# Kernel optimization log

Hardware: AMD Instinct MI355X
Metric: run time of the kernel (lower is better)

Reference implementation:

```python
import jax, jax.numpy as jnp
import numpy as np

NUM_CLASSES = 14  # centroids_pred has 14 centroids; target labels in [0,14)


def smooth(x):
    # smooth-L1: 0.5*x^2 if |x|<1 else |x|-0.5
    ax = jnp.abs(x)
    return jnp.where(ax < 1.0, 0.5 * x * x, ax - 0.5)


def setup_inputs() -> dict:
    key = jax.random.key(0)
    k1, k2, k3, k4, k5 = jax.random.split(key, 5)
    B, N, P = 32, 16384, 4096
    return {
        "displacement_pred": jax.random.normal(k1, (B, N), dtype=jnp.float32),
        "subsampled_points": jax.random.normal(k2, (B, 3, N), dtype=jnp.float32),
        "centroids_pred": jax.random.normal(k3, (B, 3, NUM_CLASSES), dtype=jnp.float32),
        "origin_points": jax.random.normal(k4, (B, 9, P), dtype=jnp.float32),
        "target": jax.random.randint(k5, (B, P), 0, NUM_CLASSES, dtype=jnp.int64),
    }


def reference(displacement_pred, subsampled_points, centroids_pred, origin_points, target):
    # origin_points: [B,9,P] -> xyz [B,P,3]
    xyz = jnp.transpose(origin_points, (0, 2, 1))[:, :, :3]
    # per-batch, per-class centroid means (get_centroids), vectorized via one-hot
    onehot = jax.nn.one_hot(target, NUM_CLASSES, dtype=xyz.dtype)       # [B,P,C]
    sums = jnp.einsum('bpc,bpd->bcd', onehot, xyz)                      # [B,C,3]
    counts = jnp.sum(onehot, axis=1)                                    # [B,C]
    cent_gt = sums / jnp.maximum(counts, 1.0)[:, :, None]               # [B,C,3]

    # distance estimate loss: nearest-GT-centroid distance per subsampled point
    sub = jnp.transpose(subsampled_points, (0, 2, 1))                   # [B,N,3]
    d2 = jnp.sum((sub[:, :, None, :] - cent_gt[:, None, :, :]) ** 2, -1)  # [B,N,C]
    dist = jnp.sqrt(jnp.min(d2, axis=-1))                               # [B,N]
    distance_loss = jnp.sum(smooth(displacement_pred - dist), axis=1)   # [B]

    # chamfer distance loss between predicted and GT centroids
    pred = jnp.transpose(centroids_pred, (0, 2, 1))                     # [B,Cp,3]
    D = jnp.sum((pred[:, :, None, :] - cent_gt[:, None, :, :]) ** 2, -1)  # [B,Cp,C]
    l1 = jnp.sum(jnp.min(D, axis=1), axis=-1)                           # [B]
    l2 = jnp.sum(jnp.min(D, axis=2), axis=-1)                           # [B]

    # separation loss: ratio of closest to 2nd-closest euclidean distance
    Dd = jnp.sqrt(D)                                                    # [B,Cp,C]
    closest2 = -jax.lax.top_k(-Dd, 2)[0]                                # [B,Cp,2] smallest two
    separation = jnp.sum(closest2[..., 0] / closest2[..., 1], axis=-1)  # [B]

    beta = 0.1
    return jnp.sum(distance_loss + l1 + l2 + beta * separation)
```

## Files before the change

kernel.cpp:

```cpp
#include <hip/hip_runtime.h>
#include <math.h>

#define NC 14
#define BB 32
#define NN 16384
#define PP 4096

#define WS_COUNTER 0
#define WS_DIST    64
#define WS_CENT    640
#define BLK_PER_B  8
#define NBLK_B     (BB * BLK_PER_B)

__global__ void centroids_kernel(const float* __restrict__ origin,
                                 const int*   __restrict__ target,
                                 float* __restrict__ ws) {
    const int b    = blockIdx.x / NC;
    const int c    = blockIdx.x % NC;
    const int tid  = threadIdx.x;
    const int lane = tid & 63;
    const int wave = tid >> 6;

    if (blockIdx.x == 0 && tid == 0) ((unsigned int*)ws)[WS_COUNTER] = 0u;

    const float* ob = origin + (size_t)b * 9 * PP;
    const int*   tb = target + (size_t)b * PP;

    float sx = 0.f, sy = 0.f, sz = 0.f, cnt = 0.f;
    const int p0 = tid * 4;
    #pragma unroll
    for (int it = 0; it < PP / 1024; ++it) {
        const int p = p0 + it * 1024;
        const int4   tv = *(const int4*)&tb[p];
        const float4 xv = *(const float4*)&ob[p];
        const float4 yv = *(const float4*)&ob[PP + p];
        const float4 zv = *(const float4*)&ob[2 * PP + p];
        float m0 = (tv.x == c) ? 1.f : 0.f;
        float m1 = (tv.y == c) ? 1.f : 0.f;
        float m2 = (tv.z == c) ? 1.f : 0.f;
        float m3 = (tv.w == c) ? 1.f : 0.f;
        sx = fmaf(m0, xv.x, fmaf(m1, xv.y, fmaf(m2, xv.z, fmaf(m3, xv.w, sx))));
        sy = fmaf(m0, yv.x, fmaf(m1, yv.y, fmaf(m2, yv.z, fmaf(m3, yv.w, sy))));
        sz = fmaf(m0, zv.x, fmaf(m1, zv.y, fmaf(m2, zv.z, fmaf(m3, zv.w, sz))));
        cnt += m0 + m1 + m2 + m3;
    }

    #pragma unroll
    for (int o = 32; o > 0; o >>= 1) {
        sx  += __shfl_down(sx, o);
        sy  += __shfl_down(sy, o);
        sz  += __shfl_down(sz, o);
        cnt += __shfl_down(cnt, o);
    }

    __shared__ float s_part[4][4];
    if (lane == 0) {
        s_part[wave][0] = sx; s_part[wave][1] = sy;
        s_part[wave][2] = sz; s_part[wave][3] = cnt;
    }
    __syncthreads();

    if (tid == 0) {
        float X = s_part[0][0] + s_part[1][0] + s_part[2][0] + s_part[3][0];
        float Y = s_part[0][1] + s_part[1][1] + s_part[2][1] + s_part[3][1];
        float Z = s_part[0][2] + s_part[1][2] + s_part[2][2] + s_part[3][2];
        float n = fmaxf(s_part[0][3] + s_part[1][3] + s_part[2][3] + s_part[3][3], 1.f);
        const int base = WS_CENT + (b * NC + c) * 3;
        ws[base + 0] = X / n;
        ws[base + 1] = Y / n;
        ws[base + 2] = Z / n;
    }
}

__global__ void distance_loss_kernel(const float* __restrict__ disp,
                                     const float* __restrict__ sub,
                                     const float* __restrict__ cpred,
                                     float* __restrict__ ws,
                                     float* __restrict__ out) {
    const int b   = blockIdx.x / BLK_PER_B;
    const int j   = blockIdx.x % BLK_PER_B;
    const int tid = threadIdx.x;

    __shared__ float s_cent[NC * 3];
    if (tid < NC * 3)
        s_cent[tid] = ws[WS_CENT + (size_t)b * NC * 3 + tid];
    __syncthreads();

    const int n0 = j * (NN / BLK_PER_B) + tid * 4;
    float sm = 0.f;
    #pragma unroll
    for (int it = 0; it < 2; ++it) {
        const int n = n0 + it * 1024;
        const float4 xv = *(const float4*)&sub[((size_t)b * 3 + 0) * NN + n];
        const float4 yv = *(const float4*)&sub[((size_t)b * 3 + 1) * NN + n];
        const float4 zv = *(const float4*)&sub[((size_t)b * 3 + 2) * NN + n];
        const float4 dv = *(const float4*)&disp[(size_t)b * NN + n];
        const float xs[4] = {xv.x, xv.y, xv.z, xv.w};
        const float ys[4] = {yv.x, yv.y, yv.z, yv.w};
        const float zs[4] = {zv.x, zv.y, zv.z, zv.w};
        const float ds[4] = {dv.x, dv.y, dv.z, dv.w};
        #pragma unroll
        for (int k = 0; k < 4; ++k) {
            float mn = 1e30f;
            #pragma unroll
            for (int c = 0; c < NC; ++c) {
                float dx = xs[k] - s_cent[c * 3 + 0];
                float dy = ys[k] - s_cent[c * 3 + 1];
                float dz = zs[k] - s_cent[c * 3 + 2];
                mn = fminf(mn, dx * dx + dy * dy + dz * dz);
            }
            float v  = ds[k] - sqrtf(mn);
            float av = fabsf(v);
            sm += (av < 1.f) ? 0.5f * v * v : (av - 0.5f);
        }
    }

    #pragma unroll
    for (int o = 32; o > 0; o >>= 1) sm += __shfl_down(sm, o);

    __shared__ float s_part[4];
    const int wave = tid >> 6;
    if ((tid & 63) == 0) s_part[wave] = sm;

    __shared__ float s_chamfer;
    if (j == 0) {
        __shared__ float s_D[NC][NC];
        if (tid < NC * NC) {
            int cp = tid / NC, c = tid % NC;
            float dx = cpred[(size_t)b * 3 * NC + 0 * NC + cp] - s_cent[c * 3 + 0];
            float dy = cpred[(size_t)b * 3 * NC + 1 * NC + cp] - s_cent[c * 3 + 1];
            float dz = cpred[(size_t)b * 3 * NC + 2 * NC + cp] - s_cent[c * 3 + 2];
            s_D[cp][c] = dx * dx + dy * dy + dz * dz;
        }
        __syncthreads();
        __shared__ float s_contrib[NC];
        if (tid < NC) {
            float mn = s_D[0][tid];
            #pragma unroll
            for (int cp = 1; cp < NC; ++cp) mn = fminf(mn, s_D[cp][tid]);
            float m1 = 1e30f, m2 = 1e30f;
            #pragma unroll
            for (int c = 0; c < NC; ++c) {
                float d = sqrtf(s_D[tid][c]);
                if (d < m1) { m2 = m1; m1 = d; }
                else if (d < m2) { m2 = d; }
            }
            s_contrib[tid] = mn + m1 * m1 + 0.1f * (m1 / m2);
        }
        __syncthreads();
        if (tid == 0) {
            float s = 0.f;
            #pragma unroll
            for (int c = 0; c < NC; ++c) s += s_contrib[c];
            s_chamfer = s;
        }
    } else if (tid == 0) {
        s_chamfer = 0.f;
    }
    __syncthreads();

    __shared__ unsigned int s_old;
    if (tid == 0) {
        ws[WS_DIST + blockIdx.x] =
            s_part[0] + s_part[1] + s_part[2] + s_part[3] + s_chamfer;
        __threadfence();
        s_old = atomicAdd((unsigned int*)ws + WS_COUNTER, 1u);
    }
    __syncthreads();

    if (s_old == NBLK_B - 1) {
        __threadfence();
        float acc = __hip_atomic_load(&ws[WS_DIST + tid], __ATOMIC_RELAXED,
                                      __HIP_MEMORY_SCOPE_AGENT);
        #pragma unroll
        for (int o = 32; o > 0; o >>= 1) acc += __shfl_down(acc, o);
        __shared__ float s_fin[4];
        if ((tid & 63) == 0) s_fin[tid >> 6] = acc;
        __syncthreads();
        if (tid == 0)
            *out = s_fin[0] + s_fin[1] + s_fin[2] + s_fin[3];
    }
}

extern "C" void kernel_launch(void* const* d_in, const int* in_sizes, int n_in,
                              void* d_out, int out_size, void* d_ws, size_t ws_size,
                              hipStream_t stream) {
    const float* disp   = (const float*)d_in[0];
    const float* sub    = (const float*)d_in[1];
    const float* cpred  = (const float*)d_in[2];
    const float* origin = (const float*)d_in[3];
    const int*   target = (const int*)d_in[4];

    float* out = (float*)d_out;
    float* ws  = (float*)d_ws;

    centroids_kernel<<<BB * NC, 256, 0, stream>>>(origin, target, ws);
    distance_loss_kernel<<<NBLK_B, 256, 0, stream>>>(disp, sub, cpred, ws, out);
}
```

Baseline: 80.02 us.

## Fuse centroid computation into distance-loss kernel and split final reduction

Each distance-loss block now computes all 14 class centroids for its batch itself, accumulating per-class sums in registers and reducing them through shared memory. This removes the separate centroids kernel and its trip through global memory. The atomic-counter last-block reduction is replaced by a small second kernel. In exchange, each batch's origin and target data is read 8 times (once per block), and every thread keeps 56 accumulators, which raises register pressure.

```diff
diff --git a/kernel.cpp b/kernel.cpp
--- a/kernel.cpp
+++ b/kernel.cpp
@@ -6,27 +6,30 @@
 #define NN 16384
 #define PP 4096
 
-#define WS_COUNTER 0
 #define WS_DIST    64
-#define WS_CENT    640
 #define BLK_PER_B  8
 #define NBLK_B     (BB * BLK_PER_B)
 
-__global__ void centroids_kernel(const float* __restrict__ origin,
-                                 const int*   __restrict__ target,
-                                 float* __restrict__ ws) {
-    const int b    = blockIdx.x / NC;
-    const int c    = blockIdx.x % NC;
+__global__ __launch_bounds__(256) void fused_loss_kernel(
+    const float* __restrict__ disp,
+    const float* __restrict__ sub,
+    const float* __restrict__ cpred,
+    const float* __restrict__ origin,
+    const int*   __restrict__ target,
+    float* __restrict__ ws) {
+    const int b    = blockIdx.x / BLK_PER_B;
+    const int j    = blockIdx.x % BLK_PER_B;
     const int tid  = threadIdx.x;
     const int lane = tid & 63;
     const int wave = tid >> 6;
 
-    if (blockIdx.x == 0 && tid == 0) ((unsigned int*)ws)[WS_COUNTER] = 0u;
-
     const float* ob = origin + (size_t)b * 9 * PP;
     const int*   tb = target + (size_t)b * PP;
 
-    float sx = 0.f, sy = 0.f, sz = 0.f, cnt = 0.f;
+    float sx[NC], sy[NC], sz[NC], cn[NC];
+    #pragma unroll
+    for (int c = 0; c < NC; ++c) { sx[c] = sy[c] = sz[c] = cn[c] = 0.f; }
+
     const int p0 = tid * 4;
     #pragma unroll
     for (int it = 0; it < PP / 1024; ++it) {
@@ -35,55 +38,56 @@
         const float4 xv = *(const float4*)&ob[p];
         const float4 yv = *(const float4*)&ob[PP + p];
         const float4 zv = *(const float4*)&ob[2 * PP + p];
-        float m0 = (tv.x == c) ? 1.f : 0.f;
-        float m1 = (tv.y == c) ? 1.f : 0.f;
-        float m2 = (tv.z == c) ? 1.f : 0.f;
-        float m3 = (tv.w == c) ? 1.f : 0.f;
-        sx = fmaf(m0, xv.x, fmaf(m1, xv.y, fmaf(m2, xv.z, fmaf(m3, xv.w, sx))));
-        sy = fmaf(m0, yv.x, fmaf(m1, yv.y, fmaf(m2, yv.z, fmaf(m3, yv.w, sy))));
-        sz = fmaf(m0, zv.x, fmaf(m1, zv.y, fmaf(m2, zv.z, fmaf(m3, zv.w, sz))));
-        cnt += m0 + m1 + m2 + m3;
+        const int   ts[4] = {tv.x, tv.y, tv.z, tv.w};
+        const float xs[4] = {xv.x, xv.y, xv.z, xv.w};
+        const float ys[4] = {yv.x, yv.y, yv.z, yv.w};
+        const float zs[4] = {zv.x, zv.y, zv.z, zv.w};
+        #pragma unroll
+        for (int k = 0; k < 4; ++k) {
+            #pragma unroll
+            for (int c = 0; c < NC; ++c) {
+                const float m = (ts[k] == c) ? 1.f : 0.f;
+                sx[c] = fmaf(m, xs[k], sx[c]);
+                sy[c] = fmaf(m, ys[k], sy[c]);
+                sz[c] = fmaf(m, zs[k], sz[c]);
+                cn[c] += m;
+            }
+        }
     }
 
     #pragma unroll
-    for (int o = 32; o > 0; o >>= 1) {
-        sx  += __shfl_down(sx, o);
-        sy  += __shfl_down(sy, o);
-        sz  += __shfl_down(sz, o);
-        cnt += __shfl_down(cnt, o);
+    for (int c = 0; c < NC; ++c) {
+        #pragma unroll
+        for (int o = 32; o > 0; o >>= 1) {
+            sx[c] += __shfl_down(sx[c], o);
+            sy[c] += __shfl_down(sy[c], o);
+            sz[c] += __shfl_down(sz[c], o);
+            cn[c] += __shfl_down(cn[c], o);
+        }
     }
 
-    __shared__ float s_part[4][4];
+    __shared__ float s_wsum[4][NC][4];
     if (lane == 0) {
-        s_part[wave][0] = sx; s_part[wave][1] = sy;
-        s_part[wave][2] = sz; s_part[wave][3] = cnt;
+        #pragma unroll
+        for (int c = 0; c < NC; ++c) {
+            s_wsum[wave][c][0] = sx[c];
+            s_wsum[wave][c][1] = sy[c];
+            s_wsum[wave][c][2] = sz[c];
+            s_wsum[wave][c][3] = cn[c];
+        }
     }
     __syncthreads();
 
-    if (tid == 0) {
-        float X = s_part[0][0] + s_part[1][0] + s_part[2][0] + s_part[3][0];
-        float Y = s_part[0][1] + s_part[1][1] + s_part[2][1] + s_part[3][1];
-        float Z = s_part[0][2] + s_part[1][2] + s_part[2][2] + s_part[3][2];
-        float n = fmaxf(s_part[0][3] + s_part[1][3] + s_part[2][3] + s_part[3][3], 1.f);
-        const int base = WS_CENT + (b * NC + c) * 3;
-        ws[base + 0] = X / n;
-        ws[base + 1] = Y / n;
-        ws[base + 2] = Z / n;
+    __shared__ float s_cent[NC * 3];
+    if (tid < NC) {
+        const float X = s_wsum[0][tid][0] + s_wsum[1][tid][0] + s_wsum[2][tid][0] + s_wsum[3][tid][0];
+        const float Y = s_wsum[0][tid][1] + s_wsum[1][tid][1] + s_wsum[2][tid][1] + s_wsum[3][tid][1];
+        const float Z = s_wsum[0][tid][2] + s_wsum[1][tid][2] + s_wsum[2][tid][2] + s_wsum[3][tid][2];
+        const float n = fmaxf(s_wsum[0][tid][3] + s_wsum[1][tid][3] + s_wsum[2][tid][3] + s_wsum[3][tid][3], 1.f);
+        s_cent[tid * 3 + 0] = X / n;
+        s_cent[tid * 3 + 1] = Y / n;
+        s_cent[tid * 3 + 2] = Z / n;
     }
-}
-
-__global__ void distance_loss_kernel(const float* __restrict__ disp,
-                                     const float* __restrict__ sub,
-                                     const float* __restrict__ cpred,
-                                     float* __restrict__ ws,
-                                     float* __restrict__ out) {
-    const int b   = blockIdx.x / BLK_PER_B;
-    const int j   = blockIdx.x % BLK_PER_B;
-    const int tid = threadIdx.x;
-
-    __shared__ float s_cent[NC * 3];
-    if (tid < NC * 3)
-        s_cent[tid] = ws[WS_CENT + (size_t)b * NC * 3 + tid];
     __syncthreads();
 
     const int n0 = j * (NN / BLK_PER_B) + tid * 4;
@@ -104,13 +108,13 @@
             float mn = 1e30f;
             #pragma unroll
             for (int c = 0; c < NC; ++c) {
-                float dx = xs[k] - s_cent[c * 3 + 0];
-                float dy = ys[k] - s_cent[c * 3 + 1];
-                float dz = zs[k] - s_cent[c * 3 + 2];
+                const float dx = xs[k] - s_cent[c * 3 + 0];
+                const float dy = ys[k] - s_cent[c * 3 + 1];
+                const float dz = zs[k] - s_cent[c * 3 + 2];
                 mn = fminf(mn, dx * dx + dy * dy + dz * dz);
             }
-            float v  = ds[k] - sqrtf(mn);
-            float av = fabsf(v);
+            const float v  = ds[k] - sqrtf(mn);
+            const float av = fabsf(v);
             sm += (av < 1.f) ? 0.5f * v * v : (av - 0.5f);
         }
     }
@@ -119,17 +123,16 @@
     for (int o = 32; o > 0; o >>= 1) sm += __shfl_down(sm, o);
 
     __shared__ float s_part[4];
-    const int wave = tid >> 6;
-    if ((tid & 63) == 0) s_part[wave] = sm;
+    if (lane == 0) s_part[wave] = sm;
 
     __shared__ float s_chamfer;
     if (j == 0) {
         __shared__ float s_D[NC][NC];
         if (tid < NC * NC) {
-            int cp = tid / NC, c = tid % NC;
-            float dx = cpred[(size_t)b * 3 * NC + 0 * NC + cp] - s_cent[c * 3 + 0];
-            float dy = cpred[(size_t)b * 3 * NC + 1 * NC + cp] - s_cent[c * 3 + 1];
-            float dz = cpred[(size_t)b * 3 * NC + 2 * NC + cp] - s_cent[c * 3 + 2];
+            const int cp = tid / NC, c = tid % NC;
+            const float dx = cpred[(size_t)b * 3 * NC + 0 * NC + cp] - s_cent[c * 3 + 0];
+            const float dy = cpred[(size_t)b * 3 * NC + 1 * NC + cp] - s_cent[c * 3 + 1];
+            const float dz = cpred[(size_t)b * 3 * NC + 2 * NC + cp] - s_cent[c * 3 + 2];
             s_D[cp][c] = dx * dx + dy * dy + dz * dz;
         }
         __syncthreads();
@@ -141,7 +144,7 @@
             float m1 = 1e30f, m2 = 1e30f;
             #pragma unroll
             for (int c = 0; c < NC; ++c) {
-                float d = sqrtf(s_D[tid][c]);
+                const float d = sqrtf(s_D[tid][c]);
                 if (d < m1) { m2 = m1; m1 = d; }
                 else if (d < m2) { m2 = d; }
             }
@@ -159,27 +162,22 @@
     }
     __syncthreads();
 
-    __shared__ unsigned int s_old;
-    if (tid == 0) {
+    if (tid == 0)
         ws[WS_DIST + blockIdx.x] =
             s_part[0] + s_part[1] + s_part[2] + s_part[3] + s_chamfer;
-        __threadfence();
-        s_old = atomicAdd((unsigned int*)ws + WS_COUNTER, 1u);
-    }
+}
+
+__global__ __launch_bounds__(256) void reduce_kernel(const float* __restrict__ ws,
+                                                     float* __restrict__ out) {
+    const int tid = threadIdx.x;
+    float acc = ws[WS_DIST + tid];
+    #pragma unroll
+    for (int o = 32; o > 0; o >>= 1) acc += __shfl_down(acc, o);
+    __shared__ float s_fin[4];
+    if ((tid & 63) == 0) s_fin[tid >> 6] = acc;
     __syncthreads();
-
-    if (s_old == NBLK_B - 1) {
-        __threadfence();
-        float acc = __hip_atomic_load(&ws[WS_DIST + tid], __ATOMIC_RELAXED,
-                                      __HIP_MEMORY_SCOPE_AGENT);
-        #pragma unroll
-        for (int o = 32; o > 0; o >>= 1) acc += __shfl_down(acc, o);
-        __shared__ float s_fin[4];
-        if ((tid & 63) == 0) s_fin[tid >> 6] = acc;
-        __syncthreads();
-        if (tid == 0)
-            *out = s_fin[0] + s_fin[1] + s_fin[2] + s_fin[3];
-    }
+    if (tid == 0)
+        *out = s_fin[0] + s_fin[1] + s_fin[2] + s_fin[3];
 }
 
 extern "C" void kernel_launch(void* const* d_in, const int* in_sizes, int n_in,
@@ -194,6 +192,6 @@
     float* out = (float*)d_out;
     float* ws  = (float*)d_ws;
 
-    centroids_kernel<<<BB * NC, 256, 0, stream>>>(origin, target, ws);
-    distance_loss_kernel<<<NBLK_B, 256, 0, stream>>>(disp, sub, cpred, ws, out);
+    fused_loss_kernel<<<NBLK_B, 256, 0, stream>>>(disp, sub, cpred, origin, target, ws);
+    reduce_kernel<<<1, 256, 0, stream>>>(ws, out);
 }
```

Measured after the change: 79.09 us. Within noise of the previous version (-1.2%).
